# Kernel tuning notes

Measured on AMD Instinct MI355X. Metric: run time of the kernel, lower is better.

The kernel has to match this reference:

```python
import jax, jax.numpy as jnp
import numpy as np

N = 50000     # nodes
E = 600000    # directed edges (avg degree 12)
F_IN = 128    # num_features
H = 128       # hidden_units
C = 16        # num_classes
G = 500       # graphs in batch


def setup_inputs() -> dict:
    key = jax.random.key(0)
    ks = jax.random.split(key, 6)
    x = jax.random.normal(ks[0], (N, F_IN), jnp.float32)
    edge_src = jax.random.randint(ks[1], (E,), 0, N, jnp.int32)
    edge_dst = jax.random.randint(ks[2], (E,), 0, N, jnp.int32)
    batch = jnp.sort(jax.random.randint(ks[3], (N,), 0, G, jnp.int32))
    W1 = jax.random.normal(ks[4], (F_IN, H), jnp.float32) / np.float32(np.sqrt(F_IN))
    b1 = jnp.zeros((H,), jnp.float32)
    W2 = jax.random.normal(ks[5], (H, C), jnp.float32) / np.float32(np.sqrt(H))
    b2 = jnp.zeros((C,), jnp.float32)
    return {"x": x, "W1": W1, "b1": b1, "W2": W2, "b2": b2,
            "edge_src": edge_src, "edge_dst": edge_dst, "batch": batch}


def _gcn_conv(x, W, b, src, dst, norm):
    # linear transform then normalized scatter-add aggregation (PyG GCNConv)
    h = x @ W                                   # [N, out]
    msg = h[src] * norm[:, None]                # [E+N, out]
    return jax.ops.segment_sum(msg, dst, num_segments=N) + b


def reference(x, W1, b1, W2, b2, edge_src, edge_dst, batch):
    # add self-loops
    loops = jnp.arange(N, dtype=edge_src.dtype)
    src = jnp.concatenate([edge_src, loops])
    dst = jnp.concatenate([edge_dst, loops])
    # symmetric normalization D^-1/2 A D^-1/2 (in-degree at targets)
    deg = jax.ops.segment_sum(jnp.ones_like(dst, jnp.float32), dst, num_segments=N)
    dis = jax.lax.rsqrt(deg)  # deg >= 1 because of self-loops
    norm = dis[src] * dis[dst]

    h = jax.nn.relu(_gcn_conv(x, W1, b1, src, dst, norm))
    h = _gcn_conv(h, W2, b2, src, dst, norm)

    # scatter_mean pooling over graphs
    counts = jax.ops.segment_sum(jnp.ones((N,), jnp.float32), batch, num_segments=G)
    pooled = jax.ops.segment_sum(h, batch, num_segments=G) / jnp.maximum(counts, 1.0)[:, None]
    return jax.nn.log_softmax(pooled, axis=1)
```

## Files before the change

### kernel.cpp

```cpp
#include <hip/hip_runtime.h>
#include <hip/hip_bf16.h>


#define NN 50000
#define EE 600000
#define FIN 128
#define HH 128
#define CC 16
#define GG 500
#define ETOT (EE + NN)
#define SBLK 196
#define WTS 140

typedef unsigned short ushort_t;
typedef unsigned int uint_t;

typedef __attribute__((ext_vector_type(8))) short bf16x8;
typedef __attribute__((ext_vector_type(8))) ushort_t u16x8;
typedef __attribute__((ext_vector_type(4))) ushort_t u16x4;
typedef __attribute__((ext_vector_type(4))) float f32x4;
typedef __attribute__((ext_vector_type(2))) float f32x2;

__device__ inline ushort_t f2bf(float f) {
    uint_t u = __float_as_uint(f);
    u = (u + 0x7FFFu + ((u >> 16) & 1u)) >> 16;
    return (ushort_t)u;
}
__device__ inline float bf2f(ushort_t b) {
    return __uint_as_float(((uint_t)b) << 16);
}
__device__ inline ushort_t f2h(float f) {
    _Float16 h = (_Float16)f; ushort_t u; __builtin_memcpy(&u, &h, 2); return u;
}
__device__ inline float h2f(ushort_t u) {
    _Float16 h; __builtin_memcpy(&h, &u, 2); return (float)h;
}

__global__ void init_kernel(int* cnt, float* pooled) {
    int i = blockIdx.x * blockDim.x + threadIdx.x;
    if (i < NN) cnt[i] = 0;
    if (i < GG * CC) pooled[i] = 0.0f;
}

__global__ void count_kernel(const int* __restrict__ edge_dst,
                             int* __restrict__ cnt, int* __restrict__ seq) {
    int idx = blockIdx.x * blockDim.x + threadIdx.x;
    if (idx < EE) seq[idx] = atomicAdd(&cnt[edge_dst[idx]], 1);
}

__global__ __launch_bounds__(256) void gemm1_kernel(const float* __restrict__ x,
                                                    const float* __restrict__ W1,
                                                    unsigned char* __restrict__ hb8) {
    __shared__ ushort_t xs[64 * 136];
    __shared__ ushort_t wt[128 * WTS];
    int t = threadIdx.x;
    int row0 = blockIdx.x * 64;
    for (int i = 0; i < 8; i++) {
        int slot = t + i * 256;
        int r = slot >> 5, k4 = slot & 31;
        int gr = row0 + r;
        float4 v = (gr < NN) ? ((const float4*)x)[gr * 32 + k4]
                             : make_float4(0.f, 0.f, 0.f, 0.f);
        u16x4 bv = { f2bf(v.x), f2bf(v.y), f2bf(v.z), f2bf(v.w) };
        *(u16x4*)(&xs[r * 136 + k4 * 4]) = bv;
    }
    for (int i = 0; i < 16; i++) {
        int idx = t + i * 256;
        int c = idx & 127, k4 = idx >> 7;
        u16x4 bv = { f2bf(W1[(4 * k4 + 0) * HH + c]),
                     f2bf(W1[(4 * k4 + 1) * HH + c]),
                     f2bf(W1[(4 * k4 + 2) * HH + c]),
                     f2bf(W1[(4 * k4 + 3) * HH + c]) };
        *(u16x4*)(&wt[c * WTS + k4 * 4]) = bv;
    }
    __syncthreads();

    int wave = t >> 6, lane = t & 63;
    int m = lane & 15, quad = lane >> 4;
    f32x4 acc[8];
    for (int ct = 0; ct < 8; ct++) acc[ct] = (f32x4)(0.0f);
    for (int ko = 0; ko < 4; ko++) {
        bf16x8 a = *(const bf16x8*)(&xs[(16 * wave + m) * 136 + ko * 32 + quad * 8]);
        for (int ct = 0; ct < 8; ct++) {
            bf16x8 b = *(const bf16x8*)(&wt[(ct * 16 + m) * WTS + ko * 32 + quad * 8]);
            acc[ct] = __builtin_amdgcn_mfma_f32_16x16x32_bf16(a, b, acc[ct], 0, 0, 0);
        }
    }
    for (int ct = 0; ct < 8; ct++) {
        int gcol = ct * 16 + m;
        for (int r = 0; r < 4; r++) {
            int grow = row0 + wave * 16 + quad * 4 + r;
            if (grow < NN) {
                int p = __builtin_amdgcn_cvt_pk_fp8_f32(acc[ct][r], 0.0f, 0, false);
                hb8[(size_t)grow * HH + gcol] = (unsigned char)(p & 0xFF);
            }
        }
    }
}

__device__ inline int block_excl_scan(int v, int t, int* total) {
    __shared__ int wsum[4];
    int lane = t & 63, wv = t >> 6;
    int inc = v;
    for (int off = 1; off < 64; off <<= 1) {
        int n = __shfl_up(inc, off);
        if (lane >= off) inc += n;
    }
    if (lane == 63) wsum[wv] = inc;
    __syncthreads();
    int off_w = 0;
    for (int w = 0; w < wv; w++) off_w += wsum[w];
    *total = wsum[0] + wsum[1] + wsum[2] + wsum[3];
    return off_w + inc - v;
}

__global__ __launch_bounds__(256) void scanA_kernel(const int* __restrict__ cnt,
                                                    int* __restrict__ rowptr,
                                                    float* __restrict__ dis,
                                                    int* __restrict__ bsum) {
    int t = threadIdx.x;
    int i = blockIdx.x * 256 + t;
    int d = 0;
    if (i < NN) {
        d = cnt[i] + 1;
        dis[i] = rsqrtf((float)d);
    }
    int total;
    int excl = block_excl_scan(d, t, &total);
    if (i < NN) rowptr[i] = excl;
    if (t == 0) bsum[blockIdx.x] = total;
}

__global__ __launch_bounds__(256) void scanBC_kernel(int* __restrict__ rowptr,
                                                     const int* __restrict__ bsum) {
    __shared__ int sb[256];
    int t = threadIdx.x;
    int v = (t < SBLK) ? bsum[t] : 0;
    int total;
    int ex = block_excl_scan(v, t, &total);
    sb[t] = ex;
    __syncthreads();
    int myoff = sb[blockIdx.x];
    int i = blockIdx.x * 256 + t;
    if (i < NN) rowptr[i] += myoff;
    if (blockIdx.x == 0 && t == 0) rowptr[NN] = ETOT;
}

__global__ void fill_kernel(const int* __restrict__ edge_src,
                            const int* __restrict__ edge_dst,
                            const float* __restrict__ dis,
                            const int* __restrict__ rowptr,
                            const int* __restrict__ seq,
                            uint_t* __restrict__ csr) {
    int idx = blockIdx.x * blockDim.x + threadIdx.x;
    if (idx < EE) {
        int s = edge_src[idx], d = edge_dst[idx];
        csr[rowptr[d] + seq[idx]] = (uint_t)s | ((uint_t)f2h(dis[s]) << 16);
    } else if (idx < ETOT) {
        int n = idx - EE;
        csr[rowptr[n + 1] - 1] = (uint_t)n | ((uint_t)f2h(dis[n]) << 16);
    }
}

__global__ __launch_bounds__(256) void agg1_kernel(const unsigned char* __restrict__ hb8,
                                                   const int* __restrict__ rowptr,
                                                   const uint_t* __restrict__ csr,
                                                   const float* __restrict__ dis,
                                                   const float* __restrict__ b1,
                                                   ushort_t* __restrict__ h1b) {
    int wave = threadIdx.x >> 6, lane = threadIdx.x & 63;
    int node = blockIdx.x * 4 + wave;
    int slot = lane >> 3, sub = lane & 7;
    int e0 = rowptr[node], e1 = rowptr[node + 1];
    float acc[16];
    for (int j = 0; j < 16; j++) acc[j] = 0.0f;
    for (int e = e0 + slot; e < e1; e += 16) {
        uint_t ent0 = csr[e];
        bool has2 = (e + 8) < e1;
        uint_t ent1 = has2 ? csr[e + 8] : ent0;
        uint4 hv0 = *(const uint4*)(hb8 + (size_t)(ent0 & 0xFFFFu) * HH + sub * 16);
        uint4 hv1 = has2 ? *(const uint4*)(hb8 + (size_t)(ent1 & 0xFFFFu) * HH + sub * 16)
                         : make_uint4(0, 0, 0, 0);
        float w0 = h2f((ushort_t)(ent0 >> 16));
        uint_t words0[4] = { hv0.x, hv0.y, hv0.z, hv0.w };
        for (int q = 0; q < 4; q++) {
            f32x2 lo = __builtin_amdgcn_cvt_pk_f32_fp8(words0[q], false);
            f32x2 hi = __builtin_amdgcn_cvt_pk_f32_fp8(words0[q], true);
            acc[q * 4 + 0] += w0 * lo[0];
            acc[q * 4 + 1] += w0 * lo[1];
            acc[q * 4 + 2] += w0 * hi[0];
            acc[q * 4 + 3] += w0 * hi[1];
        }
        if (has2) {
            float w1 = h2f((ushort_t)(ent1 >> 16));
            uint_t words1[4] = { hv1.x, hv1.y, hv1.z, hv1.w };
            for (int q = 0; q < 4; q++) {
                f32x2 lo = __builtin_amdgcn_cvt_pk_f32_fp8(words1[q], false);
                f32x2 hi = __builtin_amdgcn_cvt_pk_f32_fp8(words1[q], true);
                acc[q * 4 + 0] += w1 * lo[0];
                acc[q * 4 + 1] += w1 * lo[1];
                acc[q * 4 + 2] += w1 * hi[0];
                acc[q * 4 + 3] += w1 * hi[1];
            }
        }
    }
    for (int j = 0; j < 16; j++) {
        acc[j] += __shfl_xor(acc[j], 8);
        acc[j] += __shfl_xor(acc[j], 16);
        acc[j] += __shfl_xor(acc[j], 32);
    }
    if (slot == 0) {
        float dn = dis[node];
        const float4* b1v = (const float4*)(b1 + sub * 16);
        float4 bb[4] = { b1v[0], b1v[1], b1v[2], b1v[3] };
        const float* bbf = (const float*)bb;
        u16x8 o0, o1;
        for (int j = 0; j < 8; j++) {
            o0[j] = f2bf(fmaxf(dn * acc[j]     + bbf[j],     0.0f));
            o1[j] = f2bf(fmaxf(dn * acc[8 + j] + bbf[8 + j], 0.0f));
        }
        *(u16x8*)(h1b + (size_t)node * HH + sub * 16)     = o0;
        *(u16x8*)(h1b + (size_t)node * HH + sub * 16 + 8) = o1;
    }
}

__global__ __launch_bounds__(256) void gemm2_kernel(const ushort_t* __restrict__ h1b,
                                                    const float* __restrict__ W2,
                                                    ushort_t* __restrict__ h2b) {
    __shared__ ushort_t w2t[CC * 132];
    int t = threadIdx.x;
    for (int i = t; i < HH * CC; i += 256) {
        int k = i >> 4, m = i & 15;
        w2t[m * 132 + k] = f2bf(W2[i]);
    }
    __syncthreads();
    int wave = t >> 6, lane = t & 63;
    int m = lane & 15, quad = lane >> 4;
    int node0 = (blockIdx.x * 4 + wave) * 16;
    f32x4 acc = (f32x4)(0.0f);
    int arow = node0 + m;
    for (int ko = 0; ko < 4; ko++) {
        bf16x8 a = *(const bf16x8*)(h1b + (size_t)arow * HH + ko * 32 + quad * 8);
        bf16x8 b = *(const bf16x8*)(&w2t[m * 132 + ko * 32 + quad * 8]);
        acc = __builtin_amdgcn_mfma_f32_16x16x32_bf16(a, b, acc, 0, 0, 0);
    }
    for (int r = 0; r < 4; r++) {
        int grow = node0 + quad * 4 + r;
        h2b[(size_t)grow * CC + m] = f2bf(acc[r]);
    }
}

__global__ __launch_bounds__(1024) void agg2pool_kernel(const ushort_t* __restrict__ h2b,
                                                        const int* __restrict__ rowptr,
                                                        const uint_t* __restrict__ csr,
                                                        const float* __restrict__ dis,
                                                        const float* __restrict__ b2,
                                                        const int* __restrict__ batch,
                                                        float* __restrict__ pooled) {
    __shared__ float vals[16][16];
    __shared__ int gid[16];
    int wave = threadIdx.x >> 6, lane = threadIdx.x & 63;
    int node = blockIdx.x * 16 + wave;
    int slot = lane >> 3, sub = lane & 7;
    int e0 = rowptr[node], e1 = rowptr[node + 1];
    float a0 = 0.0f, a1 = 0.0f;
    for (int e = e0 + slot; e < e1; e += 16) {
        uint_t ent0 = csr[e];
        bool has2 = (e + 8) < e1;
        uint_t ent1 = has2 ? csr[e + 8] : ent0;
        uint_t p0 = *(const uint_t*)(h2b + (size_t)(ent0 & 0xFFFFu) * CC + sub * 2);
        uint_t p1 = has2 ? *(const uint_t*)(h2b + (size_t)(ent1 & 0xFFFFu) * CC + sub * 2) : 0;
        float w0 = h2f((ushort_t)(ent0 >> 16));
        a0 += w0 * bf2f((ushort_t)(p0 & 0xFFFFu));
        a1 += w0 * bf2f((ushort_t)(p0 >> 16));
        if (has2) {
            float w1 = h2f((ushort_t)(ent1 >> 16));
            a0 += w1 * bf2f((ushort_t)(p1 & 0xFFFFu));
            a1 += w1 * bf2f((ushort_t)(p1 >> 16));
        }
    }
    a0 += __shfl_xor(a0, 8); a0 += __shfl_xor(a0, 16); a0 += __shfl_xor(a0, 32);
    a1 += __shfl_xor(a1, 8); a1 += __shfl_xor(a1, 16); a1 += __shfl_xor(a1, 32);
    if (slot == 0) {
        float dn = dis[node];
        vals[wave][2 * sub]     = a0 * dn + b2[2 * sub];
        vals[wave][2 * sub + 1] = a1 * dn + b2[2 * sub + 1];
        if (sub == 0) gid[wave] = batch[node];
    }
    __syncthreads();
    if (threadIdx.x < 16) {
        int c = threadIdx.x;
        float run = 0.0f;
        for (int i = 0; i < 16; i++) {
            run += vals[i][c];
            if (i == 15 || gid[i + 1] != gid[i]) {
                atomicAdd(&pooled[gid[i] * CC + c], run);
                run = 0.0f;
            }
        }
    }
}

__global__ void lsm_kernel(const float* __restrict__ pooled,
                           const int* __restrict__ batch,
                           float* __restrict__ out) {
    int idx = blockIdx.x * blockDim.x + threadIdx.x;
    int g = idx >> 4, c = idx & 15;
    if (g >= GG) return;
    int lo = 0, hi = NN;
    while (lo < hi) { int mid = (lo + hi) >> 1; if (batch[mid] < g) lo = mid + 1; else hi = mid; }
    int lo2 = lo, hi2 = NN;
    while (lo2 < hi2) { int mid = (lo2 + hi2) >> 1; if (batch[mid] < g + 1) lo2 = mid + 1; else hi2 = mid; }
    float cnt = (float)(lo2 - lo);
    float v = pooled[g * CC + c] / fmaxf(cnt, 1.0f);
    float m = v;
    for (int off = 8; off >= 1; off >>= 1) m = fmaxf(m, __shfl_xor(m, off, 16));
    float s = expf(v - m);
    for (int off = 8; off >= 1; off >>= 1) s += __shfl_xor(s, off, 16);
    out[g * CC + c] = v - m - logf(s);
}

extern "C" void kernel_launch(void* const* d_in, const int* in_sizes, int n_in,
                              void* d_out, int out_size, void* d_ws, size_t ws_size,
                              hipStream_t stream) {
    const float* x  = (const float*)d_in[0];
    const float* W1 = (const float*)d_in[1];
    const float* b1 = (const float*)d_in[2];
    const float* W2 = (const float*)d_in[3];
    const float* b2 = (const float*)d_in[4];
    const int* edge_src = (const int*)d_in[5];
    const int* edge_dst = (const int*)d_in[6];
    const int* batch    = (const int*)d_in[7];
    float* out = (float*)d_out;

    char* ws = (char*)d_ws;
    size_t off = 0;
    auto alloc = [&](size_t bytes) {
        void* p = ws + off;
        off += (bytes + 255) & ~size_t(255);
        return p;
    };
    int*   cnt     = (int*)  alloc(NN * 4);
    float* dis     = (float*)alloc(NN * 4);
    int*   rowptr  = (int*)  alloc((NN + 1) * 4);
    int*   seq     = (int*)  alloc(EE * 4);
    int*   bsum    = (int*)  alloc(SBLK * 4);
    uint_t* csr    = (uint_t*)alloc((size_t)ETOT * 4);
    unsigned char* hb8 = (unsigned char*)alloc((size_t)NN * HH);
    ushort_t* h1b  = (ushort_t*)alloc((size_t)NN * HH * 2);
    ushort_t* h2b  = (ushort_t*)alloc((size_t)NN * CC * 2);
    float* pooled  = (float*)alloc(GG * CC * 4);

    const int B = 256;
    init_kernel<<<(NN + B - 1) / B, B, 0, stream>>>(cnt, pooled);
    count_kernel<<<(EE + B - 1) / B, B, 0, stream>>>(edge_dst, cnt, seq);
    gemm1_kernel<<<(NN + 63) / 64, B, 0, stream>>>(x, W1, hb8);
    scanA_kernel<<<SBLK, B, 0, stream>>>(cnt, rowptr, dis, bsum);
    scanBC_kernel<<<SBLK, B, 0, stream>>>(rowptr, bsum);
    fill_kernel<<<(ETOT + B - 1) / B, B, 0, stream>>>(edge_src, edge_dst, dis,
                                                      rowptr, seq, csr);
    agg1_kernel<<<NN / 4, B, 0, stream>>>(hb8, rowptr, csr, dis, b1, h1b);
    gemm2_kernel<<<(NN + 63) / 64, B, 0, stream>>>(h1b, W2, h2b);
    agg2pool_kernel<<<NN / 16, 1024, 0, stream>>>(h2b, rowptr, csr, dis, b2, batch, pooled);
    lsm_kernel<<<(GG * CC + B - 1) / B, B, 0, stream>>>(pooled, batch, out);
}
```

Before: 202.8 us.

## Merge graph-prep and tail stages into cooperative kernels with grid syncs

Replaces the init, count, scan, and fill kernels with one cooperative prep kernel that separates phases with grid.sync(). It also merges gemm2, aggregation with pooling, and log-softmax into one cooperative tail kernel using grid-stride loops over 256 blocks of 1024 threads. The aim is to cut kernel launch overhead and inter-kernel gaps across ten small launches. In exchange, grid-wide barriers add their own cost, and the tail stages run with a limited number of resident blocks, which may reduce parallelism.

```diff
diff --git a/kernel.cpp b/kernel.cpp
--- a/kernel.cpp
+++ b/kernel.cpp
@@ -1,5 +1,8 @@
 #include <hip/hip_runtime.h>
 #include <hip/hip_bf16.h>
+#include <hip/hip_cooperative_groups.h>
+
+namespace cg = cooperative_groups;
 
 
 #define NN 50000
@@ -11,6 +14,8 @@
 #define ETOT (EE + NN)
 #define SBLK 196
 #define WTS 140
+#define PREPB 1024
+#define TAILB 256
 
 typedef unsigned short ushort_t;
 typedef unsigned int uint_t;
@@ -36,16 +41,75 @@
     _Float16 h; __builtin_memcpy(&h, &u, 2); return (float)h;
 }
 
-__global__ void init_kernel(int* cnt, float* pooled) {
-    int i = blockIdx.x * blockDim.x + threadIdx.x;
-    if (i < NN) cnt[i] = 0;
-    if (i < GG * CC) pooled[i] = 0.0f;
-}
-
-__global__ void count_kernel(const int* __restrict__ edge_dst,
-                             int* __restrict__ cnt, int* __restrict__ seq) {
-    int idx = blockIdx.x * blockDim.x + threadIdx.x;
-    if (idx < EE) seq[idx] = atomicAdd(&cnt[edge_dst[idx]], 1);
+__device__ inline int block_excl_scan(int v, int t, int* total) {
+    __shared__ int wsum[4];
+    int lane = t & 63, wv = t >> 6;
+    int inc = v;
+    for (int off = 1; off < 64; off <<= 1) {
+        int n = __shfl_up(inc, off);
+        if (lane >= off) inc += n;
+    }
+    if (lane == 63) wsum[wv] = inc;
+    __syncthreads();
+    int off_w = 0;
+    for (int w = 0; w < wv; w++) off_w += wsum[w];
+    *total = wsum[0] + wsum[1] + wsum[2] + wsum[3];
+    return off_w + inc - v;
+}
+
+__global__ __launch_bounds__(256) void prep_kernel(const int* __restrict__ edge_src,
+                                                   const int* __restrict__ edge_dst,
+                                                   int* __restrict__ cnt,
+                                                   int* __restrict__ seq,
+                                                   float* __restrict__ dis,
+                                                   int* __restrict__ rowptr,
+                                                   int* __restrict__ bsum,
+                                                   uint_t* __restrict__ csr,
+                                                   float* __restrict__ pooled) {
+    cg::grid_group grid = cg::this_grid();
+    int t = threadIdx.x;
+    int gtid = blockIdx.x * 256 + t;
+    const int nth = PREPB * 256;
+    for (int i = gtid; i < NN; i += nth) cnt[i] = 0;
+    for (int i = gtid; i < GG * CC; i += nth) pooled[i] = 0.0f;
+    grid.sync();
+    for (int i = gtid; i < EE; i += nth) seq[i] = atomicAdd(&cnt[edge_dst[i]], 1);
+    grid.sync();
+    if (blockIdx.x < SBLK) {
+        int i = blockIdx.x * 256 + t;
+        int d = 0;
+        if (i < NN) {
+            d = cnt[i] + 1;
+            dis[i] = rsqrtf((float)d);
+        }
+        int total;
+        int excl = block_excl_scan(d, t, &total);
+        if (i < NN) rowptr[i] = excl;
+        if (t == 0) bsum[blockIdx.x] = total;
+    }
+    grid.sync();
+    if (blockIdx.x < SBLK) {
+        __shared__ int sb[256];
+        int v = (t < SBLK) ? bsum[t] : 0;
+        int total;
+        int ex = block_excl_scan(v, t, &total);
+        sb[t] = ex;
+        __syncthreads();
+        int myoff = sb[blockIdx.x];
+        int i = blockIdx.x * 256 + t;
+        if (i < NN) rowptr[i] += myoff;
+        if (blockIdx.x == 0 && t == 0) rowptr[NN] = ETOT;
+    }
+    grid.sync();
+    for (int i = gtid; i < ETOT; i += nth) {
+        if (i < EE) {
+            int s = edge_src[i], d = edge_dst[i];
+            csr[rowptr[d] + seq[i]] = (uint_t)s | ((uint_t)f2h(dis[s]) << 16);
+        } else {
+            int n = i - EE;
+            csr[rowptr[n + 1] - 1] = (uint_t)n | ((uint_t)f2h(dis[n]) << 16);
+        }
+    }
 }
 
 __global__ __launch_bounds__(256) void gemm1_kernel(const float* __restrict__ x,
@@ -95,70 +159,6 @@
                 hb8[(size_t)grow * HH + gcol] = (unsigned char)(p & 0xFF);
             }
         }
-    }
-}
-
-__device__ inline int block_excl_scan(int v, int t, int* total) {
-    __shared__ int wsum[4];
-    int lane = t & 63, wv = t >> 6;
-    int inc = v;
-    for (int off = 1; off < 64; off <<= 1) {
-        int n = __shfl_up(inc, off);
-        if (lane >= off) inc += n;
-    }
-    if (lane == 63) wsum[wv] = inc;
-    __syncthreads();
-    int off_w = 0;
-    for (int w = 0; w < wv; w++) off_w += wsum[w];
-    *total = wsum[0] + wsum[1] + wsum[2] + wsum[3];
-    return off_w + inc - v;
-}
-
-__global__ __launch_bounds__(256) void scanA_kernel(const int* __restrict__ cnt,
-                                                    int* __restrict__ rowptr,
-                                                    float* __restrict__ dis,
-                                                    int* __restrict__ bsum) {
-    int t = threadIdx.x;
-    int i = blockIdx.x * 256 + t;
-    int d = 0;
-    if (i < NN) {
-        d = cnt[i] + 1;
-        dis[i] = rsqrtf((float)d);
-    }
-    int total;
-    int excl = block_excl_scan(d, t, &total);
-    if (i < NN) rowptr[i] = excl;
-    if (t == 0) bsum[blockIdx.x] = total;
-}
-
-__global__ __launch_bounds__(256) void scanBC_kernel(int* __restrict__ rowptr,
-                                                     const int* __restrict__ bsum) {
-    __shared__ int sb[256];
-    int t = threadIdx.x;
-    int v = (t < SBLK) ? bsum[t] : 0;
-    int total;
-    int ex = block_excl_scan(v, t, &total);
-    sb[t] = ex;
-    __syncthreads();
-    int myoff = sb[blockIdx.x];
-    int i = blockIdx.x * 256 + t;
-    if (i < NN) rowptr[i] += myoff;
-    if (blockIdx.x == 0 && t == 0) rowptr[NN] = ETOT;
-}
-
-__global__ void fill_kernel(const int* __restrict__ edge_src,
-                            const int* __restrict__ edge_dst,
-                            const float* __restrict__ dis,
-                            const int* __restrict__ rowptr,
-                            const int* __restrict__ seq,
-                            uint_t* __restrict__ csr) {
-    int idx = blockIdx.x * blockDim.x + threadIdx.x;
-    if (idx < EE) {
-        int s = edge_src[idx], d = edge_dst[idx];
-        csr[rowptr[d] + seq[idx]] = (uint_t)s | ((uint_t)f2h(dis[s]) << 16);
-    } else if (idx < ETOT) {
-        int n = idx - EE;
-        csr[rowptr[n + 1] - 1] = (uint_t)n | ((uint_t)f2h(dis[n]) << 16);
     }
 }
 
@@ -224,100 +224,103 @@
     }
 }
 
-__global__ __launch_bounds__(256) void gemm2_kernel(const ushort_t* __restrict__ h1b,
+__global__ __launch_bounds__(1024) void tail_kernel(const ushort_t* __restrict__ h1b,
                                                     const float* __restrict__ W2,
-                                                    ushort_t* __restrict__ h2b) {
+                                                    ushort_t* __restrict__ h2b,
+                                                    const int* __restrict__ rowptr,
+                                                    const uint_t* __restrict__ csr,
+                                                    const float* __restrict__ dis,
+                                                    const float* __restrict__ b2,
+                                                    const int* __restrict__ batch,
+                                                    float* __restrict__ pooled,
+                                                    float* __restrict__ out) {
+    cg::grid_group grid = cg::this_grid();
     __shared__ ushort_t w2t[CC * 132];
+    __shared__ float vals[16][16];
+    __shared__ int gid[16];
     int t = threadIdx.x;
-    for (int i = t; i < HH * CC; i += 256) {
-        int k = i >> 4, m = i & 15;
-        w2t[m * 132 + k] = f2bf(W2[i]);
-    }
-    __syncthreads();
     int wave = t >> 6, lane = t & 63;
     int m = lane & 15, quad = lane >> 4;
-    int node0 = (blockIdx.x * 4 + wave) * 16;
-    f32x4 acc = (f32x4)(0.0f);
-    int arow = node0 + m;
-    for (int ko = 0; ko < 4; ko++) {
-        bf16x8 a = *(const bf16x8*)(h1b + (size_t)arow * HH + ko * 32 + quad * 8);
-        bf16x8 b = *(const bf16x8*)(&w2t[m * 132 + ko * 32 + quad * 8]);
-        acc = __builtin_amdgcn_mfma_f32_16x16x32_bf16(a, b, acc, 0, 0, 0);
-    }
-    for (int r = 0; r < 4; r++) {
-        int grow = node0 + quad * 4 + r;
-        h2b[(size_t)grow * CC + m] = f2bf(acc[r]);
-    }
-}
-
-__global__ __launch_bounds__(1024) void agg2pool_kernel(const ushort_t* __restrict__ h2b,
-                                                        const int* __restrict__ rowptr,
-                                                        const uint_t* __restrict__ csr,
-                                                        const float* __restrict__ dis,
-                                                        const float* __restrict__ b2,
-                                                        const int* __restrict__ batch,
-                                                        float* __restrict__ pooled) {
-    __shared__ float vals[16][16];
-    __shared__ int gid[16];
-    int wave = threadIdx.x >> 6, lane = threadIdx.x & 63;
-    int node = blockIdx.x * 16 + wave;
+
+    for (int i = t; i < HH * CC; i += 1024) {
+        int k = i >> 4, mm = i & 15;
+        w2t[mm * 132 + k] = f2bf(W2[i]);
+    }
+    __syncthreads();
+    for (int tile = blockIdx.x * 16 + wave; tile < NN / 16; tile += TAILB * 16) {
+        int node0 = tile * 16;
+        f32x4 acc = (f32x4)(0.0f);
+        int arow = node0 + m;
+        for (int ko = 0; ko < 4; ko++) {
+            bf16x8 a = *(const bf16x8*)(h1b + (size_t)arow * HH + ko * 32 + quad * 8);
+            bf16x8 b = *(const bf16x8*)(&w2t[m * 132 + ko * 32 + quad * 8]);
+            acc = __builtin_amdgcn_mfma_f32_16x16x32_bf16(a, b, acc, 0, 0, 0);
+        }
+        for (int r = 0; r < 4; r++) {
+            int grow = node0 + quad * 4 + r;
+            h2b[(size_t)grow * CC + m] = f2bf(acc[r]);
+        }
+    }
+    grid.sync();
+
     int slot = lane >> 3, sub = lane & 7;
-    int e0 = rowptr[node], e1 = rowptr[node + 1];
-    float a0 = 0.0f, a1 = 0.0f;
-    for (int e = e0 + slot; e < e1; e += 16) {
-        uint_t ent0 = csr[e];
-        bool has2 = (e + 8) < e1;
-        uint_t ent1 = has2 ? csr[e + 8] : ent0;
-        uint_t p0 = *(const uint_t*)(h2b + (size_t)(ent0 & 0xFFFFu) * CC + sub * 2);
-        uint_t p1 = has2 ? *(const uint_t*)(h2b + (size_t)(ent1 & 0xFFFFu) * CC + sub * 2) : 0;
-        float w0 = h2f((ushort_t)(ent0 >> 16));
-        a0 += w0 * bf2f((ushort_t)(p0 & 0xFFFFu));
-        a1 += w0 * bf2f((ushort_t)(p0 >> 16));
-        if (has2) {
-            float w1 = h2f((ushort_t)(ent1 >> 16));
-            a0 += w1 * bf2f((ushort_t)(p1 & 0xFFFFu));
-            a1 += w1 * bf2f((ushort_t)(p1 >> 16));
-        }
-    }
-    a0 += __shfl_xor(a0, 8); a0 += __shfl_xor(a0, 16); a0 += __shfl_xor(a0, 32);
-    a1 += __shfl_xor(a1, 8); a1 += __shfl_xor(a1, 16); a1 += __shfl_xor(a1, 32);
-    if (slot == 0) {
-        float dn = dis[node];
-        vals[wave][2 * sub]     = a0 * dn + b2[2 * sub];
-        vals[wave][2 * sub + 1] = a1 * dn + b2[2 * sub + 1];
-        if (sub == 0) gid[wave] = batch[node];
-    }
-    __syncthreads();
-    if (threadIdx.x < 16) {
-        int c = threadIdx.x;
-        float run = 0.0f;
-        for (int i = 0; i < 16; i++) {
-            run += vals[i][c];
-            if (i == 15 || gid[i + 1] != gid[i]) {
-                atomicAdd(&pooled[gid[i] * CC + c], run);
-                run = 0.0f;
+    for (int grp = blockIdx.x; grp < NN / 16; grp += TAILB) {
+        int node = grp * 16 + wave;
+        int e0 = rowptr[node], e1 = rowptr[node + 1];
+        float a0 = 0.0f, a1 = 0.0f;
+        for (int e = e0 + slot; e < e1; e += 16) {
+            uint_t ent0 = csr[e];
+            bool has2 = (e + 8) < e1;
+            uint_t ent1 = has2 ? csr[e + 8] : ent0;
+            uint_t p0 = *(const uint_t*)(h2b + (size_t)(ent0 & 0xFFFFu) * CC + sub * 2);
+            uint_t p1 = has2 ? *(const uint_t*)(h2b + (size_t)(ent1 & 0xFFFFu) * CC + sub * 2) : 0;
+            float w0 = h2f((ushort_t)(ent0 >> 16));
+            a0 += w0 * bf2f((ushort_t)(p0 & 0xFFFFu));
+            a1 += w0 * bf2f((ushort_t)(p0 >> 16));
+            if (has2) {
+                float w1 = h2f((ushort_t)(ent1 >> 16));
+                a0 += w1 * bf2f((ushort_t)(p1 & 0xFFFFu));
+                a1 += w1 * bf2f((ushort_t)(p1 >> 16));
             }
         }
-    }
-}
-
-__global__ void lsm_kernel(const float* __restrict__ pooled,
-                           const int* __restrict__ batch,
-                           float* __restrict__ out) {
-    int idx = blockIdx.x * blockDim.x + threadIdx.x;
+        a0 += __shfl_xor(a0, 8); a0 += __shfl_xor(a0, 16); a0 += __shfl_xor(a0, 32);
+        a1 += __shfl_xor(a1, 8); a1 += __shfl_xor(a1, 16); a1 += __shfl_xor(a1, 32);
+        if (slot == 0) {
+            float dn = dis[node];
+            vals[wave][2 * sub]     = a0 * dn + b2[2 * sub];
+            vals[wave][2 * sub + 1] = a1 * dn + b2[2 * sub + 1];
+            if (sub == 0) gid[wave] = batch[node];
+        }
+        __syncthreads();
+        if (t < 16) {
+            float run = 0.0f;
+            for (int i = 0; i < 16; i++) {
+                run += vals[i][t];
+                if (i == 15 || gid[i + 1] != gid[i]) {
+                    atomicAdd(&pooled[gid[i] * CC + t], run);
+                    run = 0.0f;
+                }
+            }
+        }
+        __syncthreads();
+    }
+    grid.sync();
+
+    int idx = blockIdx.x * 1024 + t;
     int g = idx >> 4, c = idx & 15;
-    if (g >= GG) return;
-    int lo = 0, hi = NN;
-    while (lo < hi) { int mid = (lo + hi) >> 1; if (batch[mid] < g) lo = mid + 1; else hi = mid; }
-    int lo2 = lo, hi2 = NN;
-    while (lo2 < hi2) { int mid = (lo2 + hi2) >> 1; if (batch[mid] < g + 1) lo2 = mid + 1; else hi2 = mid; }
-    float cnt = (float)(lo2 - lo);
-    float v = pooled[g * CC + c] / fmaxf(cnt, 1.0f);
-    float m = v;
-    for (int off = 8; off >= 1; off >>= 1) m = fmaxf(m, __shfl_xor(m, off, 16));
-    float s = expf(v - m);
-    for (int off = 8; off >= 1; off >>= 1) s += __shfl_xor(s, off, 16);
-    out[g * CC + c] = v - m - logf(s);
+    if (g < GG) {
+        int lo = 0, hi = NN;
+        while (lo < hi) { int mid = (lo + hi) >> 1; if (batch[mid] < g) lo = mid + 1; else hi = mid; }
+        int lo2 = lo, hi2 = NN;
+        while (lo2 < hi2) { int mid = (lo2 + hi2) >> 1; if (batch[mid] < g + 1) lo2 = mid + 1; else hi2 = mid; }
+        float cntg = (float)(lo2 - lo);
+        float v = pooled[g * CC + c] / fmaxf(cntg, 1.0f);
+        float mx = v;
+        for (int off = 8; off >= 1; off >>= 1) mx = fmaxf(mx, __shfl_xor(mx, off, 16));
+        float s = expf(v - mx);
+        for (int off = 8; off >= 1; off >>= 1) s += __shfl_xor(s, off, 16);
+        out[g * CC + c] = v - mx - logf(s);
+    }
 }
 
 extern "C" void kernel_launch(void* const* d_in, const int* in_sizes, int n_in,
@@ -351,16 +354,20 @@
     ushort_t* h2b  = (ushort_t*)alloc((size_t)NN * CC * 2);
     float* pooled  = (float*)alloc(GG * CC * 4);
 
-    const int B = 256;
-    init_kernel<<<(NN + B - 1) / B, B, 0, stream>>>(cnt, pooled);
-    count_kernel<<<(EE + B - 1) / B, B, 0, stream>>>(edge_dst, cnt, seq);
-    gemm1_kernel<<<(NN + 63) / 64, B, 0, stream>>>(x, W1, hb8);
-    scanA_kernel<<<SBLK, B, 0, stream>>>(cnt, rowptr, dis, bsum);
-    scanBC_kernel<<<SBLK, B, 0, stream>>>(rowptr, bsum);
-    fill_kernel<<<(ETOT + B - 1) / B, B, 0, stream>>>(edge_src, edge_dst, dis,
-                                                      rowptr, seq, csr);
-    agg1_kernel<<<NN / 4, B, 0, stream>>>(hb8, rowptr, csr, dis, b1, h1b);
-    gemm2_kernel<<<(NN + 63) / 64, B, 0, stream>>>(h1b, W2, h2b);
-    agg2pool_kernel<<<NN / 16, 1024, 0, stream>>>(h2b, rowptr, csr, dis, b2, batch, pooled);
-    lsm_kernel<<<(GG * CC + B - 1) / B, B, 0, stream>>>(pooled, batch, out);
-}
+    {
+        void* pa[] = { (void*)&edge_src, (void*)&edge_dst, (void*)&cnt, (void*)&seq,
+                       (void*)&dis, (void*)&rowptr, (void*)&bsum, (void*)&csr,
+                       (void*)&pooled };
+        hipLaunchCooperativeKernel((void*)prep_kernel, dim3(PREPB), dim3(256),
+                                   pa, 0, stream);
+    }
+    gemm1_kernel<<<(NN + 63) / 64, 256, 0, stream>>>(x, W1, hb8);
+    agg1_kernel<<<NN / 4, 256, 0, stream>>>(hb8, rowptr, csr, dis, b1, h1b);
+    {
+        void* pa[] = { (void*)&h1b, (void*)&W2, (void*)&h2b, (void*)&rowptr,
+                       (void*)&csr, (void*)&dis, (void*)&b2, (void*)&batch,
+                       (void*)&pooled, (void*)&out };
+        hipLaunchCooperativeKernel((void*)tail_kernel, dim3(TAILB), dim3(1024),
+                                   pa, 0, stream);
+    }
+}
```

Result: slower. 651.9 us (+221.4%).

## Merge scan kernels via grid barrier and fold log-softmax into last pooling block

Applied to the files above, without the earlier changes.

Combines the two-pass prefix scan into one kernel. Every block publishes its partial sum and then spins on a global atomic counter until all 196 blocks have arrived. The log-softmax epilogue moves into the aggregation/pooling kernel and is run by whichever block finishes last, detected through an atomic ticket. This removes two kernel launches and their gaps. In exchange it adds a spin barrier that depends on all 196 blocks being resident at once, and serializes the softmax work into a single block.

```diff
diff --git a/kernel.cpp b/kernel.cpp
--- a/kernel.cpp
+++ b/kernel.cpp
@@ -11,6 +11,7 @@
 #define ETOT (EE + NN)
 #define SBLK 196
 #define WTS 140
+#define APB (NN / 16)
 
 typedef unsigned short ushort_t;
 typedef unsigned int uint_t;
@@ -36,10 +37,11 @@
     _Float16 h; __builtin_memcpy(&h, &u, 2); return (float)h;
 }
 
-__global__ void init_kernel(int* cnt, float* pooled) {
+__global__ void init_kernel(int* cnt, float* pooled, int* flags) {
     int i = blockIdx.x * blockDim.x + threadIdx.x;
     if (i < NN) cnt[i] = 0;
     if (i < GG * CC) pooled[i] = 0.0f;
+    if (i < 2) flags[i] = 0;
 }
 
 __global__ void count_kernel(const int* __restrict__ edge_dst,
@@ -114,10 +116,12 @@
     return off_w + inc - v;
 }
 
-__global__ __launch_bounds__(256) void scanA_kernel(const int* __restrict__ cnt,
-                                                    int* __restrict__ rowptr,
-                                                    float* __restrict__ dis,
-                                                    int* __restrict__ bsum) {
+__global__ __launch_bounds__(256) void scanAB_kernel(const int* __restrict__ cnt,
+                                                     int* __restrict__ rowptr,
+                                                     float* __restrict__ dis,
+                                                     int* __restrict__ bsum,
+                                                     int* __restrict__ flags) {
+    __shared__ int sb[256];
     int t = threadIdx.x;
     int i = blockIdx.x * 256 + t;
     int d = 0;
@@ -127,22 +131,21 @@
     }
     int total;
     int excl = block_excl_scan(d, t, &total);
-    if (i < NN) rowptr[i] = excl;
-    if (t == 0) bsum[blockIdx.x] = total;
-}
-
-__global__ __launch_bounds__(256) void scanBC_kernel(int* __restrict__ rowptr,
-                                                     const int* __restrict__ bsum) {
-    __shared__ int sb[256];
-    int t = threadIdx.x;
-    int v = (t < SBLK) ? bsum[t] : 0;
-    int total;
-    int ex = block_excl_scan(v, t, &total);
+    if (t == 0) {
+        bsum[blockIdx.x] = total;
+        __threadfence();
+        atomicAdd(&flags[0], 1);
+        while (__hip_atomic_load(&flags[0], __ATOMIC_ACQUIRE,
+                                 __HIP_MEMORY_SCOPE_AGENT) < SBLK) {}
+    }
+    __syncthreads();
+    int v = (t < SBLK) ? __hip_atomic_load(&bsum[t], __ATOMIC_RELAXED,
+                                           __HIP_MEMORY_SCOPE_AGENT) : 0;
+    int tot2;
+    int ex = block_excl_scan(v, t, &tot2);
     sb[t] = ex;
     __syncthreads();
-    int myoff = sb[blockIdx.x];
-    int i = blockIdx.x * 256 + t;
-    if (i < NN) rowptr[i] += myoff;
+    if (i < NN) rowptr[i] = excl + sb[blockIdx.x];
     if (blockIdx.x == 0 && t == 0) rowptr[NN] = ETOT;
 }
 
@@ -256,10 +259,14 @@
                                                         const float* __restrict__ dis,
                                                         const float* __restrict__ b2,
                                                         const int* __restrict__ batch,
-                                                        float* __restrict__ pooled) {
+                                                        float* __restrict__ pooled,
+                                                        int* __restrict__ flags,
+                                                        float* __restrict__ out) {
     __shared__ float vals[16][16];
     __shared__ int gid[16];
-    int wave = threadIdx.x >> 6, lane = threadIdx.x & 63;
+    __shared__ int lastflag;
+    int t = threadIdx.x;
+    int wave = t >> 6, lane = t & 63;
     int node = blockIdx.x * 16 + wave;
     int slot = lane >> 3, sub = lane & 7;
     int e0 = rowptr[node], e1 = rowptr[node + 1];
@@ -288,36 +295,40 @@
         if (sub == 0) gid[wave] = batch[node];
     }
     __syncthreads();
-    if (threadIdx.x < 16) {
-        int c = threadIdx.x;
+    if (t < 16) {
         float run = 0.0f;
         for (int i = 0; i < 16; i++) {
-            run += vals[i][c];
+            run += vals[i][t];
             if (i == 15 || gid[i + 1] != gid[i]) {
-                atomicAdd(&pooled[gid[i] * CC + c], run);
+                atomicAdd(&pooled[gid[i] * CC + t], run);
                 run = 0.0f;
             }
         }
     }
-}
-
-__global__ void lsm_kernel(const float* __restrict__ pooled,
-                           const int* __restrict__ batch,
-                           float* __restrict__ out) {
-    int idx = blockIdx.x * blockDim.x + threadIdx.x;
-    int g = idx >> 4, c = idx & 15;
-    if (g >= GG) return;
-    int lo = 0, hi = NN;
-    while (lo < hi) { int mid = (lo + hi) >> 1; if (batch[mid] < g) lo = mid + 1; else hi = mid; }
-    int lo2 = lo, hi2 = NN;
-    while (lo2 < hi2) { int mid = (lo2 + hi2) >> 1; if (batch[mid] < g + 1) lo2 = mid + 1; else hi2 = mid; }
-    float cnt = (float)(lo2 - lo);
-    float v = pooled[g * CC + c] / fmaxf(cnt, 1.0f);
-    float m = v;
-    for (int off = 8; off >= 1; off >>= 1) m = fmaxf(m, __shfl_xor(m, off, 16));
-    float s = expf(v - m);
-    for (int off = 8; off >= 1; off >>= 1) s += __shfl_xor(s, off, 16);
-    out[g * CC + c] = v - m - logf(s);
+    __syncthreads();
+    if (t == 0) {
+        __threadfence();
+        int prev = atomicAdd(&flags[1], 1);
+        lastflag = (prev == APB - 1);
+    }
+    __syncthreads();
+    if (!lastflag) return;
+    for (int idx = t; idx < GG * CC; idx += 1024) {
+        int g = idx >> 4, c = idx & 15;
+        int lo = 0, hi = NN;
+        while (lo < hi) { int mid = (lo + hi) >> 1; if (batch[mid] < g) lo = mid + 1; else hi = mid; }
+        int lo2 = lo, hi2 = NN;
+        while (lo2 < hi2) { int mid = (lo2 + hi2) >> 1; if (batch[mid] < g + 1) lo2 = mid + 1; else hi2 = mid; }
+        float cntg = (float)(lo2 - lo);
+        float pv = __hip_atomic_load(&pooled[g * CC + c], __ATOMIC_RELAXED,
+                                     __HIP_MEMORY_SCOPE_AGENT);
+        float v = pv / fmaxf(cntg, 1.0f);
+        float mx = v;
+        for (int off = 8; off >= 1; off >>= 1) mx = fmaxf(mx, __shfl_xor(mx, off, 16));
+        float s = expf(v - mx);
+        for (int off = 8; off >= 1; off >>= 1) s += __shfl_xor(s, off, 16);
+        out[g * CC + c] = v - mx - logf(s);
+    }
 }
 
 extern "C" void kernel_launch(void* const* d_in, const int* in_sizes, int n_in,
@@ -345,6 +356,7 @@
     int*   rowptr  = (int*)  alloc((NN + 1) * 4);
     int*   seq     = (int*)  alloc(EE * 4);
     int*   bsum    = (int*)  alloc(SBLK * 4);
+    int*   flags   = (int*)  alloc(2 * 4);
     uint_t* csr    = (uint_t*)alloc((size_t)ETOT * 4);
     unsigned char* hb8 = (unsigned char*)alloc((size_t)NN * HH);
     ushort_t* h1b  = (ushort_t*)alloc((size_t)NN * HH * 2);
@@ -352,15 +364,14 @@
     float* pooled  = (float*)alloc(GG * CC * 4);
 
     const int B = 256;
-    init_kernel<<<(NN + B - 1) / B, B, 0, stream>>>(cnt, pooled);
+    init_kernel<<<(NN + B - 1) / B, B, 0, stream>>>(cnt, pooled, flags);
     count_kernel<<<(EE + B - 1) / B, B, 0, stream>>>(edge_dst, cnt, seq);
     gemm1_kernel<<<(NN + 63) / 64, B, 0, stream>>>(x, W1, hb8);
-    scanA_kernel<<<SBLK, B, 0, stream>>>(cnt, rowptr, dis, bsum);
-    scanBC_kernel<<<SBLK, B, 0, stream>>>(rowptr, bsum);
+    scanAB_kernel<<<SBLK, B, 0, stream>>>(cnt, rowptr, dis, bsum, flags);
     fill_kernel<<<(ETOT + B - 1) / B, B, 0, stream>>>(edge_src, edge_dst, dis,
                                                       rowptr, seq, csr);
     agg1_kernel<<<NN / 4, B, 0, stream>>>(hb8, rowptr, csr, dis, b1, h1b);
     gemm2_kernel<<<(NN + 63) / 64, B, 0, stream>>>(h1b, W2, h2b);
-    agg2pool_kernel<<<NN / 16, 1024, 0, stream>>>(h2b, rowptr, csr, dis, b2, batch, pooled);
-    lsm_kernel<<<(GG * CC + B - 1) / B, B, 0, stream>>>(pooled, batch, out);
-}
+    agg2pool_kernel<<<APB, 1024, 0, stream>>>(h2b, rowptr, csr, dis, b2, batch,
+                                              pooled, flags, out);
+}
```

New measurement: 316.2 us. 1.56x slower.
